# Optimization experiments

Measured on AMD Instinct MI355X. Metric: run time of the kernel, lower is better.

Reference implementation:

```python
import jax, jax.numpy as jnp
import numpy as np

B, C, H, W = 2, 512, 48, 48
HEADS = 8
REDUCTION = 4
DPH = max(C // REDUCTION // HEADS, 1)   # 16
TOTAL = DPH * HEADS                      # 128
EPS_NORM = 1e-12
EPS_BN = 1e-5


def setup_inputs() -> dict:
    key = jax.random.key(0)
    ks = jax.random.split(key, 6)
    x = jax.random.normal(ks[0], (B, C, H, W), dtype=jnp.float32)
    # 1x1 convs stored as [out_ch, in_ch] matrices
    w_qkv = jax.random.normal(ks[1], (3 * TOTAL, C), dtype=jnp.float32) * (1.0 / np.sqrt(C))
    w_out = jax.random.normal(ks[2], (C, TOTAL), dtype=jnp.float32) * (1.0 / np.sqrt(TOTAL))
    temperature = jnp.ones((HEADS, 1, 1), dtype=jnp.float32)
    bn_gamma = jnp.ones((C,), dtype=jnp.float32)
    bn_beta = jnp.zeros((C,), dtype=jnp.float32)
    return {"x": x, "w_qkv": w_qkv, "temperature": temperature,
            "w_out": w_out, "bn_gamma": bn_gamma, "bn_beta": bn_beta}


def _l2norm(t):
    # F.normalize(t, dim=-1): t / max(||t||_2, eps)
    n = jnp.sqrt(jnp.sum(t * t, axis=-1, keepdims=True))
    return t / jnp.maximum(n, EPS_NORM)


def reference(x, w_qkv, temperature, w_out, bn_gamma, bn_beta):
    b, c, h, w = x.shape
    n = h * w
    # qkv 1x1 conv: [b, 3*TOTAL, h, w]
    qkv = jnp.einsum('bchw,oc->bohw', x, w_qkv)
    q, k, v = jnp.split(qkv, 3, axis=1)
    # [b, heads, dph, n] -> [b, heads, n, dph]
    def heads_tokens(t):
        return t.reshape(b, HEADS, DPH, n).transpose(0, 1, 3, 2)
    q = _l2norm(heads_tokens(q))
    k = _l2norm(heads_tokens(k))
    v = heads_tokens(v)
    # [b, heads, n, n]
    attn = jnp.einsum('bhnd,bhmd->bhnm', q, k) * temperature[None]
    attn = jax.nn.softmax(attn, axis=-1)
    out = jnp.einsum('bhnm,bhmd->bhnd', attn, v)          # [b, heads, n, dph]
    out = out.transpose(0, 1, 3, 2).reshape(b, TOTAL, h, w)
    # project_out: 1x1 conv then BatchNorm2d (training-mode batch stats)
    out = jnp.einsum('bthw,ct->bchw', out, w_out)
    mean = jnp.mean(out, axis=(0, 2, 3))
    var = jnp.mean((out - mean[None, :, None, None]) ** 2, axis=(0, 2, 3))
    out = (out - mean[None, :, None, None]) * jax.lax.rsqrt(var + EPS_BN)[None, :, None, None]
    out = out * bn_gamma[None, :, None, None] + bn_beta[None, :, None, None]
    return out
```

## Files before the change

kernel.cpp:

```cpp
#include <hip/hip_runtime.h>

#define NB 2
#define CC 512
#define NN 2304
#define NH 8
#define DD 16
#define TT 128
#define O3 384

typedef __attribute__((ext_vector_type(4))) float f32x4;
typedef __attribute__((ext_vector_type(8))) __bf16 bf16x8;
typedef __attribute__((ext_vector_type(4))) __bf16 bf16x4;
typedef __attribute__((ext_vector_type(2))) __bf16 bf16x2;
typedef __attribute__((ext_vector_type(4))) _Float16 f16x4;
typedef __attribute__((ext_vector_type(2))) __fp16 hf16x2;

union hf2pair {
    hf16x2 h[2];
    f16x4  v;
};

#define OFF_XT 0u
#define OFF_WQ 4718592u
#define OFF_WO 5111808u
#define OFF_Q  5242880u
#define OFF_K  6422528u
#define OFF_VT 7602176u
#define OFF_AO 8781824u
#define OFF_PRE 9961472u

__global__ __launch_bounds__(256) void k0_convert(
    const float* __restrict__ x, const float* __restrict__ wqkv,
    const float* __restrict__ wout,
    __bf16* __restrict__ xT, __bf16* __restrict__ wqb, __bf16* __restrict__ wob)
{
    int bid = blockIdx.x;
    int t = threadIdx.x;
    if (bid < 576) {
        __shared__ float tile[64][65];
        int b = bid / 288, rem = bid % 288;
        int nt = rem / 8, cb = rem % 8;
        int n0 = nt * 64, c0 = cb * 64;
        int nq = (t & 15) * 4;
        int cs = t >> 4;
#pragma unroll
        for (int i = 0; i < 4; i++) {
            int c = i * 16 + cs;
            f32x4 v = *(const f32x4*)(x + (size_t)(b * CC + c0 + c) * NN + n0 + nq);
            tile[c][nq + 0] = v[0];
            tile[c][nq + 1] = v[1];
            tile[c][nq + 2] = v[2];
            tile[c][nq + 3] = v[3];
        }
        __syncthreads();
        int cq = (t & 15) * 4;
        int ns = t >> 4;
#pragma unroll
        for (int i = 0; i < 4; i++) {
            int n = i * 16 + ns;
            bf16x4 pk;
            pk[0] = (__bf16)tile[cq + 0][n];
            pk[1] = (__bf16)tile[cq + 1][n];
            pk[2] = (__bf16)tile[cq + 2][n];
            pk[3] = (__bf16)tile[cq + 3][n];
            *(bf16x4*)(xT + (size_t)(b * NN + n0 + n) * CC + c0 + cq) = pk;
        }
    } else {
        int wid = bid - 576;
#pragma unroll
        for (int i = 0; i < 4; i++) {
            int jq = wid * 256 + t + i * 16384;
            int j = jq * 4;
            f32x4 v = (j < O3 * CC) ? *(const f32x4*)(wqkv + j)
                                    : *(const f32x4*)(wout + (j - O3 * CC));
            bf16x4 pk;
            pk[0] = (__bf16)v[0]; pk[1] = (__bf16)v[1];
            pk[2] = (__bf16)v[2]; pk[3] = (__bf16)v[3];
            if (j < O3 * CC) *(bf16x4*)(wqb + j) = pk;
            else             *(bf16x4*)(wob + (j - O3 * CC)) = pk;
        }
    }
}

__global__ __launch_bounds__(256) void k1_qkv(
    const __bf16* __restrict__ xT, const __bf16* __restrict__ wqb,
    _Float16* __restrict__ Q, _Float16* __restrict__ K, _Float16* __restrict__ VT)
{
    int ob = blockIdx.x, nt = blockIdx.y, b = blockIdx.z;
    int lane = threadIdx.x & 63, wave = threadIdx.x >> 6;
    int quad = lane >> 4, col = lane & 15;
    int n0 = nt * 64 + wave * 16;
    int o0 = ob * 64;

    f32x4 acc0 = {0.f,0.f,0.f,0.f}, acc1 = {0.f,0.f,0.f,0.f};
    f32x4 acc2 = {0.f,0.f,0.f,0.f}, acc3 = {0.f,0.f,0.f,0.f};

    const __bf16* arow  = xT + (size_t)(b * NN + n0 + col) * CC + quad * 8;
    const __bf16* brow0 = wqb + (size_t)(o0 + col) * CC + quad * 8;
    const __bf16* brow1 = brow0 + 16 * CC;
    const __bf16* brow2 = brow0 + 32 * CC;
    const __bf16* brow3 = brow0 + 48 * CC;

    bf16x8 a  = *(const bf16x8*)(arow);
    bf16x8 w0 = *(const bf16x8*)(brow0);
    bf16x8 w1 = *(const bf16x8*)(brow1);
    bf16x8 w2 = *(const bf16x8*)(brow2);
    bf16x8 w3 = *(const bf16x8*)(brow3);
#pragma unroll
    for (int ks = 0; ks < 16; ks++) {
        bf16x8 an, wn0, wn1, wn2, wn3;
        if (ks < 15) {
            an  = *(const bf16x8*)(arow + (ks + 1) * 32);
            wn0 = *(const bf16x8*)(brow0 + (ks + 1) * 32);
            wn1 = *(const bf16x8*)(brow1 + (ks + 1) * 32);
            wn2 = *(const bf16x8*)(brow2 + (ks + 1) * 32);
            wn3 = *(const bf16x8*)(brow3 + (ks + 1) * 32);
        }
        acc0 = __builtin_amdgcn_mfma_f32_16x16x32_bf16(a, w0, acc0, 0, 0, 0);
        acc1 = __builtin_amdgcn_mfma_f32_16x16x32_bf16(a, w1, acc1, 0, 0, 0);
        acc2 = __builtin_amdgcn_mfma_f32_16x16x32_bf16(a, w2, acc2, 0, 0, 0);
        acc3 = __builtin_amdgcn_mfma_f32_16x16x32_bf16(a, w3, acc3, 0, 0, 0);
        a = an; w0 = wn0; w1 = wn1; w2 = wn2; w3 = wn3;
    }

#pragma unroll
    for (int s = 0; s < 4; s++) {
        int oc = o0 + s * 16 + col;
        int d = oc & 15, h = (oc >> 4) & 7, kind = oc >> 7;
        f32x4 v = (s == 0) ? acc0 : (s == 1) ? acc1 : (s == 2) ? acc2 : acc3;
        if (kind < 2) {
            float ss0 = v[0] * v[0], ss1 = v[1] * v[1], ss2 = v[2] * v[2], ss3 = v[3] * v[3];
#pragma unroll
            for (int m = 1; m < 16; m <<= 1) {
                ss0 += __shfl_xor(ss0, m);
                ss1 += __shfl_xor(ss1, m);
                ss2 += __shfl_xor(ss2, m);
                ss3 += __shfl_xor(ss3, m);
            }
            v[0] *= 1.0f / fmaxf(sqrtf(ss0), 1e-12f);
            v[1] *= 1.0f / fmaxf(sqrtf(ss1), 1e-12f);
            v[2] *= 1.0f / fmaxf(sqrtf(ss2), 1e-12f);
            v[3] *= 1.0f / fmaxf(sqrtf(ss3), 1e-12f);
            _Float16* dst = (kind == 0 ? Q : K) + (size_t)(b * NH + h) * NN * DD;
#pragma unroll
            for (int r = 0; r < 4; r++) {
                int n = n0 + quad * 4 + r;
                dst[(size_t)n * DD + d] = (_Float16)v[r];
            }
        } else {
            f16x4 pk;
#pragma unroll
            for (int r = 0; r < 4; r++) pk[r] = (_Float16)v[r];
            int n = n0 + quad * 4;
            *(f16x4*)(VT + (size_t)((b * NH + h) * DD + d) * NN + n) = pk;
        }
    }
}

__global__ __launch_bounds__(512) void k2_attn(
    const _Float16* __restrict__ Q, const _Float16* __restrict__ K,
    const _Float16* __restrict__ VT, const float* __restrict__ temp,
    __bf16* __restrict__ AO)
{
    __shared__ float Osh[8][16][64];
    __shared__ float Lsh[8][64];

    int qt = blockIdx.x, bh = blockIdx.y;
    int lane = threadIdx.x & 63, wave = threadIdx.x >> 6;
    int quad = lane >> 4, col = lane & 15;
    int kbase = wave * 288;
    int qbase = qt * 64;

    const _Float16* Qb = Q + (size_t)bh * NN * DD;
    float tl2 = temp[bh & 7] * 1.4426950408889634f;
    _Float16 tl2h = (_Float16)tl2;

    f16x4 qf0 = *(const f16x4*)(Qb + (size_t)(qbase +  0 + col) * DD + quad * 4);
    f16x4 qf1 = *(const f16x4*)(Qb + (size_t)(qbase + 16 + col) * DD + quad * 4);
    f16x4 qf2 = *(const f16x4*)(Qb + (size_t)(qbase + 32 + col) * DD + quad * 4);
    f16x4 qf3 = *(const f16x4*)(Qb + (size_t)(qbase + 48 + col) * DD + quad * 4);
#pragma unroll
    for (int j = 0; j < 4; j++) {
        qf0[j] *= tl2h; qf1[j] *= tl2h; qf2[j] *= tl2h; qf3[j] *= tl2h;
    }

    f32x4 oa0 = {0.f,0.f,0.f,0.f}, oa1 = {0.f,0.f,0.f,0.f};
    f32x4 oa2 = {0.f,0.f,0.f,0.f}, oa3 = {0.f,0.f,0.f,0.f};
    float la0 = 0.f, la1 = 0.f, la2 = 0.f, la3 = 0.f;
    const f32x4 zc = {0.f,0.f,0.f,0.f};

    const _Float16* kp = K + (size_t)bh * NN * DD + (size_t)(kbase + col) * DD + quad * 4;
    const _Float16* vp = VT + (size_t)bh * DD * NN + (size_t)col * NN + kbase + quad * 4;

    f16x4 kfa = *(const f16x4*)(kp);
    f16x4 kfb = *(const f16x4*)(kp + 16 * DD);
    f16x4 vfa = *(const f16x4*)(vp);
    f16x4 vfb = *(const f16x4*)(vp + 16);

#define K2_CHUNK(KF, VF)                                                        \
    {                                                                           \
        f32x4 s0 = __builtin_amdgcn_mfma_f32_16x16x16f16(KF, qf0, zc, 0, 0, 0); \
        f32x4 s1 = __builtin_amdgcn_mfma_f32_16x16x16f16(KF, qf1, zc, 0, 0, 0); \
        f32x4 s2 = __builtin_amdgcn_mfma_f32_16x16x16f16(KF, qf2, zc, 0, 0, 0); \
        f32x4 s3 = __builtin_amdgcn_mfma_f32_16x16x16f16(KF, qf3, zc, 0, 0, 0); \
        float e00 = __builtin_amdgcn_exp2f(s0[0]), e01 = __builtin_amdgcn_exp2f(s0[1]); \
        float e02 = __builtin_amdgcn_exp2f(s0[2]), e03 = __builtin_amdgcn_exp2f(s0[3]); \
        float e10 = __builtin_amdgcn_exp2f(s1[0]), e11 = __builtin_amdgcn_exp2f(s1[1]); \
        float e12 = __builtin_amdgcn_exp2f(s1[2]), e13 = __builtin_amdgcn_exp2f(s1[3]); \
        float e20 = __builtin_amdgcn_exp2f(s2[0]), e21 = __builtin_amdgcn_exp2f(s2[1]); \
        float e22 = __builtin_amdgcn_exp2f(s2[2]), e23 = __builtin_amdgcn_exp2f(s2[3]); \
        float e30 = __builtin_amdgcn_exp2f(s3[0]), e31 = __builtin_amdgcn_exp2f(s3[1]); \
        float e32 = __builtin_amdgcn_exp2f(s3[2]), e33 = __builtin_amdgcn_exp2f(s3[3]); \
        la0 += (e00 + e01) + (e02 + e03);                                       \
        la1 += (e10 + e11) + (e12 + e13);                                       \
        la2 += (e20 + e21) + (e22 + e23);                                       \
        la3 += (e30 + e31) + (e32 + e33);                                       \
        hf2pair u0, u1, u2, u3;                                                 \
        u0.h[0] = __builtin_amdgcn_cvt_pkrtz(e00, e01);                         \
        u0.h[1] = __builtin_amdgcn_cvt_pkrtz(e02, e03);                         \
        u1.h[0] = __builtin_amdgcn_cvt_pkrtz(e10, e11);                         \
        u1.h[1] = __builtin_amdgcn_cvt_pkrtz(e12, e13);                         \
        u2.h[0] = __builtin_amdgcn_cvt_pkrtz(e20, e21);                         \
        u2.h[1] = __builtin_amdgcn_cvt_pkrtz(e22, e23);                         \
        u3.h[0] = __builtin_amdgcn_cvt_pkrtz(e30, e31);                         \
        u3.h[1] = __builtin_amdgcn_cvt_pkrtz(e32, e33);                         \
        oa0 = __builtin_amdgcn_mfma_f32_16x16x16f16(VF, u0.v, oa0, 0, 0, 0);    \
        oa1 = __builtin_amdgcn_mfma_f32_16x16x16f16(VF, u1.v, oa1, 0, 0, 0);    \
        oa2 = __builtin_amdgcn_mfma_f32_16x16x16f16(VF, u2.v, oa2, 0, 0, 0);    \
        oa3 = __builtin_amdgcn_mfma_f32_16x16x16f16(VF, u3.v, oa3, 0, 0, 0);    \
    }

    for (int g = 0; g < 9; ++g) {
        f16x4 kna, knb, vna, vnb;
        if (g < 8) {
            kna = *(const f16x4*)(kp + 32 * DD);
            knb = *(const f16x4*)(kp + 48 * DD);
            vna = *(const f16x4*)(vp + 32);
            vnb = *(const f16x4*)(vp + 48);
        }
        K2_CHUNK(kfa, vfa)
        K2_CHUNK(kfb, vfb)
        kfa = kna; kfb = knb; vfa = vna; vfb = vnb;
        kp += 32 * DD; vp += 32;
    }
#undef K2_CHUNK

    la0 += __shfl_xor(la0, 16); la0 += __shfl_xor(la0, 32);
    la1 += __shfl_xor(la1, 16); la1 += __shfl_xor(la1, 32);
    la2 += __shfl_xor(la2, 16); la2 += __shfl_xor(la2, 32);
    la3 += __shfl_xor(la3, 16); la3 += __shfl_xor(la3, 32);

#pragma unroll
    for (int r = 0; r < 4; ++r) {
        Osh[wave][quad * 4 + r][ 0 + col] = oa0[r];
        Osh[wave][quad * 4 + r][16 + col] = oa1[r];
        Osh[wave][quad * 4 + r][32 + col] = oa2[r];
        Osh[wave][quad * 4 + r][48 + col] = oa3[r];
    }
    float lv = (quad == 0) ? la0 : (quad == 1) ? la1 : (quad == 2) ? la2 : la3;
    Lsh[wave][quad * 16 + col] = lv;
    __syncthreads();

    int t = threadIdx.x;
    int q = t & 63, dg = t >> 6;
    float l = 0.f;
#pragma unroll
    for (int w = 0; w < 8; ++w) l += Lsh[w][q];
    float inv = 1.0f / l;
    float o0 = 0.f, o1 = 0.f;
#pragma unroll
    for (int w = 0; w < 8; ++w) {
        o0 += Osh[w][dg * 2 + 0][q];
        o1 += Osh[w][dg * 2 + 1][q];
    }
    int b = bh >> 3, h = bh & 7;
    bf16x2 pk;
    pk[0] = (__bf16)(o0 * inv);
    pk[1] = (__bf16)(o1 * inv);
    *(bf16x2*)(AO + (size_t)(b * NN + qbase + q) * TT + h * DD + dg * 2) = pk;
}

__global__ __launch_bounds__(256) void k3_proj(
    const __bf16* __restrict__ AO, const __bf16* __restrict__ wob,
    __bf16* __restrict__ pre)
{
    int cb = blockIdx.x, nt = blockIdx.y, b = blockIdx.z;
    int lane = threadIdx.x & 63, wave = threadIdx.x >> 6;
    int quad = lane >> 4, col = lane & 15;
    int n0 = nt * 64 + wave * 16, c0 = cb * 32;

    f32x4 acc0 = {0.f, 0.f, 0.f, 0.f};
    f32x4 acc1 = {0.f, 0.f, 0.f, 0.f};

    const __bf16* ab = AO + (size_t)(b * NN + n0 + col) * TT + quad * 8;
    const __bf16* wb0 = wob + (size_t)(c0 + col) * TT + quad * 8;
    const __bf16* wb1 = wb0 + 16 * TT;
#pragma unroll
    for (int ks = 0; ks < 4; ks++) {
        bf16x8 a  = *(const bf16x8*)(ab + ks * 32);
        bf16x8 w0 = *(const bf16x8*)(wb0 + ks * 32);
        bf16x8 w1 = *(const bf16x8*)(wb1 + ks * 32);
        acc0 = __builtin_amdgcn_mfma_f32_16x16x32_bf16(a, w0, acc0, 0, 0, 0);
        acc1 = __builtin_amdgcn_mfma_f32_16x16x32_bf16(a, w1, acc1, 0, 0, 0);
    }
#pragma unroll
    for (int s = 0; s < 2; s++) {
        int c = c0 + s * 16 + col;
        f32x4 v = (s == 0) ? acc0 : acc1;
        bf16x4 pk;
        pk[0] = (__bf16)v[0]; pk[1] = (__bf16)v[1];
        pk[2] = (__bf16)v[2]; pk[3] = (__bf16)v[3];
        *(bf16x4*)(pre + (size_t)(b * CC + c) * NN + n0 + quad * 4) = pk;
    }
}

__global__ __launch_bounds__(256) void k4_bn(
    const __bf16* __restrict__ pre, float* __restrict__ out,
    const float* __restrict__ gamma, const float* __restrict__ beta)
{
    int c = blockIdx.x;
    int t = threadIdx.x;
    float vals[2][9];
    float s = 0.f, q = 0.f;
#pragma unroll
    for (int b = 0; b < 2; b++) {
        const __bf16* base = pre + (size_t)(b * CC + c) * NN;
#pragma unroll
        for (int r = 0; r < 2; r++) {
            bf16x4 x4 = *(const bf16x4*)(base + r * 1024 + t * 4);
#pragma unroll
            for (int j = 0; j < 4; j++) {
                float v = (float)x4[j];
                vals[b][r * 4 + j] = v; s += v; q += v * v;
            }
        }
        float v = (float)base[2048 + t];
        vals[b][8] = v; s += v; q += v * v;
    }
#pragma unroll
    for (int m = 1; m < 64; m <<= 1) { s += __shfl_xor(s, m); q += __shfl_xor(q, m); }
    __shared__ float rs[4], rq[4];
    int lane = t & 63, wave = t >> 6;
    if (lane == 0) { rs[wave] = s; rq[wave] = q; }
    __syncthreads();
    s = rs[0] + rs[1] + rs[2] + rs[3];
    q = rq[0] + rq[1] + rq[2] + rq[3];
    float mean = s * (1.0f / 4608.0f);
    float var = q * (1.0f / 4608.0f) - mean * mean;
    float sc = rsqrtf(var + 1e-5f) * gamma[c];
    float sh = beta[c] - mean * sc;
#pragma unroll
    for (int b = 0; b < 2; b++) {
        float* obase = out + (size_t)(b * CC + c) * NN;
#pragma unroll
        for (int r = 0; r < 2; r++) {
            f32x4 o;
#pragma unroll
            for (int j = 0; j < 4; j++) o[j] = vals[b][r * 4 + j] * sc + sh;
            *(f32x4*)(obase + r * 1024 + t * 4) = o;
        }
        obase[2048 + t] = vals[b][8] * sc + sh;
    }
}

extern "C" void kernel_launch(void* const* d_in, const int* in_sizes, int n_in,
                              void* d_out, int out_size, void* d_ws, size_t ws_size,
                              hipStream_t stream) {
    const float* x     = (const float*)d_in[0];
    const float* wqkv  = (const float*)d_in[1];
    const float* temp  = (const float*)d_in[2];
    const float* wout  = (const float*)d_in[3];
    const float* gamma = (const float*)d_in[4];
    const float* beta  = (const float*)d_in[5];
    float* out = (float*)d_out;
    char* ws = (char*)d_ws;

    __bf16* xT  = (__bf16*)(ws + OFF_XT);
    __bf16* wqb = (__bf16*)(ws + OFF_WQ);
    __bf16* wob = (__bf16*)(ws + OFF_WO);
    _Float16* Q  = (_Float16*)(ws + OFF_Q);
    _Float16* K  = (_Float16*)(ws + OFF_K);
    _Float16* VT = (_Float16*)(ws + OFF_VT);
    __bf16* AO  = (__bf16*)(ws + OFF_AO);
    __bf16* PRE = (__bf16*)(ws + OFF_PRE);

    k0_convert<<<640, 256, 0, stream>>>(x, wqkv, wout, xT, wqb, wob);
    k1_qkv<<<dim3(6, 36, 2), 256, 0, stream>>>(xT, wqb, Q, K, VT);
    k2_attn<<<dim3(36, 16), 512, 0, stream>>>(Q, K, VT, temp, AO);
    k3_proj<<<dim3(16, 36, 2), 256, 0, stream>>>(AO, wob, PRE);
    k4_bn<<<512, 256, 0, stream>>>(PRE, out, gamma, beta);
}
```

Before: 127.7 us.

## Fuse BatchNorm statistics into projection epilogue via atomics

The projection kernel now computes per-channel partial sums and sums of squares from its fp32 accumulators, reduces them across the wave with shuffles, and adds them atomically into workspace buffers. The conversion kernel zeroes those buffers first. The BN kernel no longer does its own reduction: it reads the precomputed statistics and normalizes one (batch, channel) row per block, using twice as many blocks. This removes the reduction and block barrier from the final pass, in exchange for atomic contention in the projection epilogue and nondeterministic summation order.

Measured after the change: 131.5 us. 3.0% more time.

```diff
diff --git a/kernel.cpp b/kernel.cpp
--- a/kernel.cpp
+++ b/kernel.cpp
@@ -28,11 +28,14 @@
 #define OFF_VT 7602176u
 #define OFF_AO 8781824u
 #define OFF_PRE 9961472u
+#define OFF_RS 14680064u
+#define OFF_RQ 14682112u
 
 __global__ __launch_bounds__(256) void k0_convert(
     const float* __restrict__ x, const float* __restrict__ wqkv,
     const float* __restrict__ wout,
-    __bf16* __restrict__ xT, __bf16* __restrict__ wqb, __bf16* __restrict__ wob)
+    __bf16* __restrict__ xT, __bf16* __restrict__ wqb, __bf16* __restrict__ wob,
+    float* __restrict__ RS, float* __restrict__ RQ)
 {
     int bid = blockIdx.x;
     int t = threadIdx.x;
@@ -67,6 +70,8 @@
         }
     } else {
         int wid = bid - 576;
+        int z = wid * 256 + t;
+        if (z < 512) { RS[z] = 0.f; RQ[z] = 0.f; }
 #pragma unroll
         for (int i = 0; i < 4; i++) {
             int jq = wid * 256 + t + i * 16384;
@@ -282,7 +287,7 @@
 
 __global__ __launch_bounds__(256) void k3_proj(
     const __bf16* __restrict__ AO, const __bf16* __restrict__ wob,
-    __bf16* __restrict__ pre)
+    __bf16* __restrict__ pre, float* __restrict__ RS, float* __restrict__ RQ)
 {
     int cb = blockIdx.x, nt = blockIdx.y, b = blockIdx.z;
     int lane = threadIdx.x & 63, wave = threadIdx.x >> 6;
@@ -311,56 +316,41 @@
         pk[0] = (__bf16)v[0]; pk[1] = (__bf16)v[1];
         pk[2] = (__bf16)v[2]; pk[3] = (__bf16)v[3];
         *(bf16x4*)(pre + (size_t)(b * CC + c) * NN + n0 + quad * 4) = pk;
+        float ps = (v[0] + v[1]) + (v[2] + v[3]);
+        float pq = (v[0] * v[0] + v[1] * v[1]) + (v[2] * v[2] + v[3] * v[3]);
+        ps += __shfl_xor(ps, 16); ps += __shfl_xor(ps, 32);
+        pq += __shfl_xor(pq, 16); pq += __shfl_xor(pq, 32);
+        if (quad == 0) {
+            atomicAdd(&RS[c], ps);
+            atomicAdd(&RQ[c], pq);
+        }
     }
 }
 
 __global__ __launch_bounds__(256) void k4_bn(
-    const __bf16* __restrict__ pre, float* __restrict__ out,
+    const __bf16* __restrict__ pre, const float* __restrict__ RS,
+    const float* __restrict__ RQ, float* __restrict__ out,
     const float* __restrict__ gamma, const float* __restrict__ beta)
 {
-    int c = blockIdx.x;
+    int row = blockIdx.x;
+    int c = row & 511;
     int t = threadIdx.x;
-    float vals[2][9];
-    float s = 0.f, q = 0.f;
-#pragma unroll
-    for (int b = 0; b < 2; b++) {
-        const __bf16* base = pre + (size_t)(b * CC + c) * NN;
-#pragma unroll
-        for (int r = 0; r < 2; r++) {
-            bf16x4 x4 = *(const bf16x4*)(base + r * 1024 + t * 4);
-#pragma unroll
-            for (int j = 0; j < 4; j++) {
-                float v = (float)x4[j];
-                vals[b][r * 4 + j] = v; s += v; q += v * v;
-            }
-        }
-        float v = (float)base[2048 + t];
-        vals[b][8] = v; s += v; q += v * v;
-    }
-#pragma unroll
-    for (int m = 1; m < 64; m <<= 1) { s += __shfl_xor(s, m); q += __shfl_xor(q, m); }
-    __shared__ float rs[4], rq[4];
-    int lane = t & 63, wave = t >> 6;
-    if (lane == 0) { rs[wave] = s; rq[wave] = q; }
-    __syncthreads();
-    s = rs[0] + rs[1] + rs[2] + rs[3];
-    q = rq[0] + rq[1] + rq[2] + rq[3];
-    float mean = s * (1.0f / 4608.0f);
-    float var = q * (1.0f / 4608.0f) - mean * mean;
+    float mean = RS[c] * (1.0f / 4608.0f);
+    float var  = RQ[c] * (1.0f / 4608.0f) - mean * mean;
     float sc = rsqrtf(var + 1e-5f) * gamma[c];
     float sh = beta[c] - mean * sc;
-#pragma unroll
-    for (int b = 0; b < 2; b++) {
-        float* obase = out + (size_t)(b * CC + c) * NN;
-#pragma unroll
-        for (int r = 0; r < 2; r++) {
-            f32x4 o;
-#pragma unroll
-            for (int j = 0; j < 4; j++) o[j] = vals[b][r * 4 + j] * sc + sh;
-            *(f32x4*)(obase + r * 1024 + t * 4) = o;
-        }
-        obase[2048 + t] = vals[b][8] * sc + sh;
-    }
+
+    const __bf16* base = pre + (size_t)row * NN;
+    float* obase = out + (size_t)row * NN;
+#pragma unroll
+    for (int r = 0; r < 2; r++) {
+        bf16x4 x4 = *(const bf16x4*)(base + r * 1024 + t * 4);
+        f32x4 o;
+#pragma unroll
+        for (int j = 0; j < 4; j++) o[j] = (float)x4[j] * sc + sh;
+        *(f32x4*)(obase + r * 1024 + t * 4) = o;
+    }
+    obase[2048 + t] = (float)base[2048 + t] * sc + sh;
 }
 
 extern "C" void kernel_launch(void* const* d_in, const int* in_sizes, int n_in,
@@ -383,10 +373,12 @@
     _Float16* VT = (_Float16*)(ws + OFF_VT);
     __bf16* AO  = (__bf16*)(ws + OFF_AO);
     __bf16* PRE = (__bf16*)(ws + OFF_PRE);
-
-    k0_convert<<<640, 256, 0, stream>>>(x, wqkv, wout, xT, wqb, wob);
+    float*  RS  = (float*)(ws + OFF_RS);
+    float*  RQ  = (float*)(ws + OFF_RQ);
+
+    k0_convert<<<640, 256, 0, stream>>>(x, wqkv, wout, xT, wqb, wob, RS, RQ);
     k1_qkv<<<dim3(6, 36, 2), 256, 0, stream>>>(xT, wqb, Q, K, VT);
     k2_attn<<<dim3(36, 16), 512, 0, stream>>>(Q, K, VT, temp, AO);
-    k3_proj<<<dim3(16, 36, 2), 256, 0, stream>>>(AO, wob, PRE);
-    k4_bn<<<512, 256, 0, stream>>>(PRE, out, gamma, beta);
-}
+    k3_proj<<<dim3(16, 36, 2), 256, 0, stream>>>(AO, wob, PRE, RS, RQ);
+    k4_bn<<<1024, 256, 0, stream>>>(PRE, RS, RQ, out, gamma, beta);
+}
```
